# Kernel tuning notes

Hardware: AMD Instinct MI355X
Metric: run time of the kernel (lower is better)

## Reference

```python
import jax, jax.numpy as jnp
import numpy as np

B = 64        # number of graphs in the batch
NPG = 1024    # nodes per graph (uniform batch_num_nodes)
N = B * NPG   # total nodes = 65536
D = 512       # input feature dim
DEG = 32      # average degree
K = 0.5       # keep-percent
DROP = NPG - int(np.ceil(K * NPG))  # number of lowest-score nodes zeroed per graph


def setup_inputs() -> dict:
    key = jax.random.key(0)
    k1, k2, k3, k4 = jax.random.split(key, 4)
    features = jax.random.normal(k1, (N, D), dtype=jnp.float32)
    # edges constrained inside each graph's node block (batched DGL graph is block-diagonal)
    offsets = (jnp.arange(B, dtype=jnp.int64) * NPG)[:, None]
    src = (jax.random.randint(k2, (B, NPG * DEG), 0, NPG, dtype=jnp.int64) + offsets).reshape(-1)
    dst = (jax.random.randint(k3, (B, NPG * DEG), 0, NPG, dtype=jnp.int64) + offsets).reshape(-1)
    # GraphConv(input_dim=D, out=1) parameters (glorot-ish scale)
    weight = jax.random.normal(k4, (D, 1), dtype=jnp.float32) * (1.0 / np.sqrt(D))
    bias = jnp.zeros((1,), dtype=jnp.float32)
    return {"features": features, "src": src, "dst": dst, "weight": weight, "bias": bias}


def reference(features, src, dst, weight, bias):
    # --- GraphConv(D -> 1, norm=True, bias=True, activation=relu) ---
    # old-DGL norm=True: symmetric normalization with in-degrees, norm=deg^-0.5 (0 for isolated)
    deg = jnp.zeros((N,), features.dtype).at[dst].add(1.0)
    norm = jnp.where(deg > 0, deg ** -0.5, 0.0)[:, None]          # [N,1]
    # in_feats > out_feats: project first, then aggregate scalars
    h = (features @ weight) * norm                                # [N,1]
    agg = jnp.zeros_like(h).at[dst].add(h[src])                   # sum over in-edges
    w = jax.nn.relu(agg * norm + bias)                            # [N,1] scores
    # --- per-graph top-k masking: zero the DROP smallest scores in each graph ---
    wb = w.reshape(B, NPG)
    ranks = jnp.argsort(jnp.argsort(wb, axis=1), axis=1)          # rank 0 = smallest
    wb = jnp.where(ranks < DROP, jnp.zeros((), wb.dtype), wb)
    # --- elementwise gating of features by (masked) scores ---
    return features * wb.reshape(N, 1)
```

## Files before the change

kernel.cpp:

```cpp
#include <hip/hip_runtime.h>

#define NTOT 65536
#define DIM  512
#define BGR  64
#define NPG  1024
#define DROPN 512
#define SLICES 8

typedef float vf4 __attribute__((ext_vector_type(4)));

__global__ __launch_bounds__(256) void matvec_kernel(
        const float* __restrict__ X, const float* __restrict__ W,
        float* __restrict__ p) {
    const int lane = threadIdx.x & 63;
    const int nw   = (gridDim.x * blockDim.x) >> 6;
    const int wid  = (blockIdx.x * blockDim.x + threadIdx.x) >> 6;
    const vf4* wr = (const vf4*)W;
    const vf4 w0 = wr[lane], w1 = wr[lane + 64];
    for (int row = wid; row < NTOT; row += 2 * nw) {
        const int row2 = row + nw;
        const vf4* xr0 = (const vf4*)(X + (size_t)row  * DIM);
        const vf4* xr1 = (const vf4*)(X + (size_t)row2 * DIM);
        vf4 a0 = xr0[lane], a1 = xr0[lane + 64];
        vf4 b0 = xr1[lane], b1 = xr1[lane + 64];
        vf4 m0 = a0 * w0 + a1 * w1;
        vf4 m1 = b0 * w0 + b1 * w1;
        float s0 = m0[0] + m0[1] + m0[2] + m0[3];
        float s1 = m1[0] + m1[1] + m1[2] + m1[3];
        #pragma unroll
        for (int off = 32; off > 0; off >>= 1) {
            s0 += __shfl_down(s0, off, 64);
            s1 += __shfl_down(s1, off, 64);
        }
        if (lane == 0) { p[row] = s0; p[row2] = s1; }
    }
}

__global__ __launch_bounds__(256) void deg_partial_kernel(
        const int* __restrict__ dst, float* __restrict__ deg, int epg) {
    __shared__ int dl[NPG];
    const int g = blockIdx.x & (BGR - 1);
    const int slice = blockIdx.x >> 6;
    const int nbase = g * NPG;
    const int eps = epg / SLICES;
    for (int i = threadIdx.x; i < NPG; i += 256) dl[i] = 0;
    __syncthreads();
    const int4* d4 = (const int4*)(dst + (size_t)g * epg + (size_t)slice * eps);
    const int n4 = eps >> 2;
    for (int i = threadIdx.x; i < n4; i += 256) {
        int4 d = d4[i];
        atomicAdd(&dl[d.x - nbase], 1);
        atomicAdd(&dl[d.y - nbase], 1);
        atomicAdd(&dl[d.z - nbase], 1);
        atomicAdd(&dl[d.w - nbase], 1);
    }
    __syncthreads();
    for (int i = threadIdx.x; i < NPG; i += 256) {
        int c = dl[i];
        if (c) atomicAdd(&deg[nbase + i], (float)c);
    }
}

__global__ __launch_bounds__(256) void hn_kernel(
        const float* __restrict__ p, const float* __restrict__ deg,
        float* __restrict__ hn) {
    int i = blockIdx.x * blockDim.x + threadIdx.x;
    if (i < NTOT) {
        float d = deg[i];
        float nrm = d > 0.f ? (1.0f / sqrtf(d)) : 0.f;
        hn[i] = p[i] * nrm;
    }
}

__global__ __launch_bounds__(256) void agg_partial_kernel(
        const int* __restrict__ src, const int* __restrict__ dst,
        const float* __restrict__ hn, float* __restrict__ agg, int epg) {
    __shared__ float al[NPG];
    __shared__ float hl[NPG];
    const int g = blockIdx.x & (BGR - 1);
    const int slice = blockIdx.x >> 6;
    const int nbase = g * NPG;
    const int eps = epg / SLICES;
    for (int i = threadIdx.x; i < NPG; i += 256) {
        al[i] = 0.f;
        hl[i] = hn[nbase + i];
    }
    __syncthreads();
    const int4* s4 = (const int4*)(src + (size_t)g * epg + (size_t)slice * eps);
    const int4* d4 = (const int4*)(dst + (size_t)g * epg + (size_t)slice * eps);
    const int n4 = eps >> 2;
    for (int i = threadIdx.x; i < n4; i += 256) {
        int4 s = s4[i];
        int4 d = d4[i];
        atomicAdd(&al[d.x - nbase], hl[s.x - nbase]);
        atomicAdd(&al[d.y - nbase], hl[s.y - nbase]);
        atomicAdd(&al[d.z - nbase], hl[s.z - nbase]);
        atomicAdd(&al[d.w - nbase], hl[s.w - nbase]);
    }
    __syncthreads();
    for (int i = threadIdx.x; i < NPG; i += 256) {
        float v = al[i];
        if (v != 0.f) atomicAdd(&agg[nbase + i], v);
    }
}

__global__ __launch_bounds__(1024) void topk_kernel(
        const float* __restrict__ agg, const float* __restrict__ deg,
        const float* __restrict__ bias, float* __restrict__ gate) {
    __shared__ unsigned long long keys[NPG];
    __shared__ float wv[NPG];
    const int g = blockIdx.x;
    const int t = threadIdx.x;
    const int nbase = g * NPG;
    float d = deg[nbase + t];
    float nrm = d > 0.f ? (1.0f / sqrtf(d)) : 0.f;
    float w = agg[nbase + t] * nrm + bias[0];
    w = w > 0.f ? w : 0.f;
    wv[t] = w;
    keys[t] = ((unsigned long long)__float_as_uint(w) << 32) | (unsigned int)t;
    __syncthreads();
    for (int k = 2; k <= NPG; k <<= 1) {
        for (int j = k >> 1; j > 0; j >>= 1) {
            int ixj = t ^ j;
            if (ixj > t) {
                unsigned long long a = keys[t], c = keys[ixj];
                bool up = ((t & k) == 0);
                if ((a > c) == up) { keys[t] = c; keys[ixj] = a; }
            }
            __syncthreads();
        }
    }
    int idx = (int)(keys[t] & 0xffffffffull);
    gate[nbase + idx] = (t < DROPN) ? 0.f : wv[idx];
}

__global__ __launch_bounds__(256) void gate_kernel(
        const float* __restrict__ X, const float* __restrict__ gate,
        float* __restrict__ out) {
    const int lane = threadIdx.x & 63;
    const int nw   = (gridDim.x * blockDim.x) >> 6;
    const int wid  = (blockIdx.x * blockDim.x + threadIdx.x) >> 6;
    for (int row = wid; row < NTOT; row += nw) {
        float g = gate[__builtin_amdgcn_readfirstlane(row)];
        vf4* o = (vf4*)(out + (size_t)row * DIM);
        if (g == 0.f) {
            vf4 z = (vf4){0.f, 0.f, 0.f, 0.f};
            __builtin_nontemporal_store(z, &o[lane]);
            __builtin_nontemporal_store(z, &o[lane + 64]);
        } else {
            const vf4* xr = (const vf4*)(X + (size_t)row * DIM);
            vf4 a = xr[lane] * g;
            vf4 c = xr[lane + 64] * g;
            __builtin_nontemporal_store(a, &o[lane]);
            __builtin_nontemporal_store(c, &o[lane + 64]);
        }
    }
}

extern "C" void kernel_launch(void* const* d_in, const int* in_sizes, int n_in,
                              void* d_out, int out_size, void* d_ws, size_t ws_size,
                              hipStream_t stream) {
    const float* X    = (const float*)d_in[0];
    const int*   src  = (const int*)d_in[1];
    const int*   dst  = (const int*)d_in[2];
    const float* W    = (const float*)d_in[3];
    const float* bias = (const float*)d_in[4];
    float* out = (float*)d_out;
    int E   = in_sizes[1];
    int epg = E / BGR;

    float* ws   = (float*)d_ws;
    float* p    = ws;
    float* hn   = ws + 1 * NTOT;
    float* deg  = ws + 2 * NTOT;
    float* agg  = ws + 3 * NTOT;
    float* gate = ws + 4 * NTOT;

    hipMemsetAsync(deg, 0, 2 * NTOT * sizeof(float), stream);

    matvec_kernel<<<2048, 256, 0, stream>>>(X, W, p);
    deg_partial_kernel<<<BGR * SLICES, 256, 0, stream>>>(dst, deg, epg);
    hn_kernel<<<NTOT / 256, 256, 0, stream>>>(p, deg, hn);
    agg_partial_kernel<<<BGR * SLICES, 256, 0, stream>>>(src, dst, hn, agg, epg);
    topk_kernel<<<BGR, 1024, 0, stream>>>(agg, deg, bias, gate);
    gate_kernel<<<2048, 256, 0, stream>>>(X, gate, out);
}
```

Before: 284.9 us.

## Fuse pipeline into four kernels, replace atomics with slice partials, register bitonic sort

Merges the matvec and degree-count kernels into one launch, with separate block ranges for each job. Degree and aggregation partials are now written per slice and summed by the consumer, which removes the memset, the global atomics and the separate hn kernel. The top-k bitonic sort keeps keys in registers and uses wavefront shuffles for strides below 64, and the gate kernel switches from nontemporal stores to plain stores. This cuts launches and barriers, but adds reads of the partial buffers, and the change of store type may alter cache behaviour on the large output.

Result: no change. 280.2 us (-1.6%).

```diff
diff --git a/kernel.cpp b/kernel.cpp
--- a/kernel.cpp
+++ b/kernel.cpp
@@ -6,84 +6,81 @@
 #define NPG  1024
 #define DROPN 512
 #define SLICES 8
+#define MV_BLOCKS 2048
 
 typedef float vf4 __attribute__((ext_vector_type(4)));
+typedef unsigned long long u64;
 
-__global__ __launch_bounds__(256) void matvec_kernel(
+__global__ __launch_bounds__(256) void k1_matvec_deg(
         const float* __restrict__ X, const float* __restrict__ W,
-        float* __restrict__ p) {
-    const int lane = threadIdx.x & 63;
-    const int nw   = (gridDim.x * blockDim.x) >> 6;
-    const int wid  = (blockIdx.x * blockDim.x + threadIdx.x) >> 6;
-    const vf4* wr = (const vf4*)W;
-    const vf4 w0 = wr[lane], w1 = wr[lane + 64];
-    for (int row = wid; row < NTOT; row += 2 * nw) {
-        const int row2 = row + nw;
-        const vf4* xr0 = (const vf4*)(X + (size_t)row  * DIM);
-        const vf4* xr1 = (const vf4*)(X + (size_t)row2 * DIM);
-        vf4 a0 = xr0[lane], a1 = xr0[lane + 64];
-        vf4 b0 = xr1[lane], b1 = xr1[lane + 64];
-        vf4 m0 = a0 * w0 + a1 * w1;
-        vf4 m1 = b0 * w0 + b1 * w1;
-        float s0 = m0[0] + m0[1] + m0[2] + m0[3];
-        float s1 = m1[0] + m1[1] + m1[2] + m1[3];
-        #pragma unroll
-        for (int off = 32; off > 0; off >>= 1) {
-            s0 += __shfl_down(s0, off, 64);
-            s1 += __shfl_down(s1, off, 64);
+        const int* __restrict__ dst,
+        float* __restrict__ p, int* __restrict__ deg_part, int epg) {
+    __shared__ int dl[NPG];
+    if (blockIdx.x < MV_BLOCKS) {
+        const int lane = threadIdx.x & 63;
+        const int wid  = (blockIdx.x * 256 + threadIdx.x) >> 6;
+        const int nw   = (MV_BLOCKS * 256) >> 6;
+        const vf4* wr = (const vf4*)W;
+        const vf4 w0 = wr[lane], w1 = wr[lane + 64];
+        for (int row = wid; row < NTOT; row += 2 * nw) {
+            const int row2 = row + nw;
+            const vf4* xr0 = (const vf4*)(X + (size_t)row  * DIM);
+            const vf4* xr1 = (const vf4*)(X + (size_t)row2 * DIM);
+            vf4 a0 = xr0[lane], a1 = xr0[lane + 64];
+            vf4 b0 = xr1[lane], b1 = xr1[lane + 64];
+            vf4 m0 = a0 * w0 + a1 * w1;
+            vf4 m1 = b0 * w0 + b1 * w1;
+            float s0 = m0[0] + m0[1] + m0[2] + m0[3];
+            float s1 = m1[0] + m1[1] + m1[2] + m1[3];
+            #pragma unroll
+            for (int off = 32; off > 0; off >>= 1) {
+                s0 += __shfl_down(s0, off, 64);
+                s1 += __shfl_down(s1, off, 64);
+            }
+            if (lane == 0) { p[row] = s0; p[row2] = s1; }
         }
-        if (lane == 0) { p[row] = s0; p[row2] = s1; }
+    } else {
+        const int b = blockIdx.x - MV_BLOCKS;
+        const int g = b & (BGR - 1);
+        const int slice = b >> 6;
+        const int nbase = g * NPG;
+        const int eps = epg / SLICES;
+        for (int i = threadIdx.x; i < NPG; i += 256) dl[i] = 0;
+        __syncthreads();
+        const int4* d4 = (const int4*)(dst + (size_t)g * epg + (size_t)slice * eps);
+        const int n4 = eps >> 2;
+        for (int i = threadIdx.x; i < n4; i += 256) {
+            int4 d = d4[i];
+            atomicAdd(&dl[d.x - nbase], 1);
+            atomicAdd(&dl[d.y - nbase], 1);
+            atomicAdd(&dl[d.z - nbase], 1);
+            atomicAdd(&dl[d.w - nbase], 1);
+        }
+        __syncthreads();
+        int* out = deg_part + (size_t)slice * NTOT + nbase;
+        for (int i = threadIdx.x; i < NPG; i += 256) out[i] = dl[i];
     }
 }
 
-__global__ __launch_bounds__(256) void deg_partial_kernel(
-        const int* __restrict__ dst, float* __restrict__ deg, int epg) {
-    __shared__ int dl[NPG];
-    const int g = blockIdx.x & (BGR - 1);
-    const int slice = blockIdx.x >> 6;
-    const int nbase = g * NPG;
-    const int eps = epg / SLICES;
-    for (int i = threadIdx.x; i < NPG; i += 256) dl[i] = 0;
-    __syncthreads();
-    const int4* d4 = (const int4*)(dst + (size_t)g * epg + (size_t)slice * eps);
-    const int n4 = eps >> 2;
-    for (int i = threadIdx.x; i < n4; i += 256) {
-        int4 d = d4[i];
-        atomicAdd(&dl[d.x - nbase], 1);
-        atomicAdd(&dl[d.y - nbase], 1);
-        atomicAdd(&dl[d.z - nbase], 1);
-        atomicAdd(&dl[d.w - nbase], 1);
-    }
-    __syncthreads();
-    for (int i = threadIdx.x; i < NPG; i += 256) {
-        int c = dl[i];
-        if (c) atomicAdd(&deg[nbase + i], (float)c);
-    }
-}
-
-__global__ __launch_bounds__(256) void hn_kernel(
-        const float* __restrict__ p, const float* __restrict__ deg,
-        float* __restrict__ hn) {
-    int i = blockIdx.x * blockDim.x + threadIdx.x;
-    if (i < NTOT) {
-        float d = deg[i];
-        float nrm = d > 0.f ? (1.0f / sqrtf(d)) : 0.f;
-        hn[i] = p[i] * nrm;
-    }
-}
-
-__global__ __launch_bounds__(256) void agg_partial_kernel(
+__global__ __launch_bounds__(256) void k2_agg(
         const int* __restrict__ src, const int* __restrict__ dst,
-        const float* __restrict__ hn, float* __restrict__ agg, int epg) {
+        const float* __restrict__ p, const int* __restrict__ deg_part,
+        float* __restrict__ agg_part, float* __restrict__ norm_out, int epg) {
+    __shared__ float hl[NPG];
     __shared__ float al[NPG];
-    __shared__ float hl[NPG];
-    const int g = blockIdx.x & (BGR - 1);
-    const int slice = blockIdx.x >> 6;
+    const int b = blockIdx.x;
+    const int g = b & (BGR - 1);
+    const int slice = b >> 6;
     const int nbase = g * NPG;
     const int eps = epg / SLICES;
     for (int i = threadIdx.x; i < NPG; i += 256) {
+        int d = 0;
+        #pragma unroll
+        for (int s = 0; s < SLICES; s++) d += deg_part[(size_t)s * NTOT + nbase + i];
+        float nrm = d > 0 ? (1.0f / sqrtf((float)d)) : 0.f;
+        hl[i] = p[nbase + i] * nrm;
         al[i] = 0.f;
-        hl[i] = hn[nbase + i];
+        if (slice == 0) norm_out[nbase + i] = nrm;
     }
     __syncthreads();
     const int4* s4 = (const int4*)(src + (size_t)g * epg + (size_t)slice * eps);
@@ -98,61 +95,64 @@
         atomicAdd(&al[d.w - nbase], hl[s.w - nbase]);
     }
     __syncthreads();
-    for (int i = threadIdx.x; i < NPG; i += 256) {
-        float v = al[i];
-        if (v != 0.f) atomicAdd(&agg[nbase + i], v);
-    }
+    float* out = agg_part + (size_t)slice * NTOT + nbase;
+    for (int i = threadIdx.x; i < NPG; i += 256) out[i] = al[i];
 }
 
-__global__ __launch_bounds__(1024) void topk_kernel(
-        const float* __restrict__ agg, const float* __restrict__ deg,
+__global__ __launch_bounds__(1024) void k3_topk(
+        const float* __restrict__ agg_part, const float* __restrict__ norm,
         const float* __restrict__ bias, float* __restrict__ gate) {
-    __shared__ unsigned long long keys[NPG];
-    __shared__ float wv[NPG];
+    __shared__ u64 sk[NPG];
     const int g = blockIdx.x;
     const int t = threadIdx.x;
     const int nbase = g * NPG;
-    float d = deg[nbase + t];
-    float nrm = d > 0.f ? (1.0f / sqrtf(d)) : 0.f;
-    float w = agg[nbase + t] * nrm + bias[0];
+    float a = 0.f;
+    #pragma unroll
+    for (int s = 0; s < SLICES; s++) a += agg_part[(size_t)s * NTOT + nbase + t];
+    float w = a * norm[nbase + t] + bias[0];
     w = w > 0.f ? w : 0.f;
-    wv[t] = w;
-    keys[t] = ((unsigned long long)__float_as_uint(w) << 32) | (unsigned int)t;
-    __syncthreads();
+    u64 key = ((u64)__float_as_uint(w) << 32) | (unsigned int)t;
+
     for (int k = 2; k <= NPG; k <<= 1) {
-        for (int j = k >> 1; j > 0; j >>= 1) {
-            int ixj = t ^ j;
-            if (ixj > t) {
-                unsigned long long a = keys[t], c = keys[ixj];
-                bool up = ((t & k) == 0);
-                if ((a > c) == up) { keys[t] = c; keys[ixj] = a; }
-            }
+        const bool up = ((t & k) == 0);
+        for (int j = k >> 1; j >= 64; j >>= 1) {
+            sk[t] = key;
             __syncthreads();
+            u64 partner = sk[t ^ j];
+            __syncthreads();
+            bool takeMin = (((t & j) == 0) == up);
+            key = takeMin ? (key < partner ? key : partner)
+                          : (key > partner ? key : partner);
+        }
+        for (int j = ((k >> 1) < 32 ? (k >> 1) : 32); j >= 1; j >>= 1) {
+            u64 partner = (u64)__shfl_xor((long long)key, j, 64);
+            bool takeMin = (((t & j) == 0) == up);
+            key = takeMin ? (key < partner ? key : partner)
+                          : (key > partner ? key : partner);
         }
     }
-    int idx = (int)(keys[t] & 0xffffffffull);
-    gate[nbase + idx] = (t < DROPN) ? 0.f : wv[idx];
+    int idx = (int)(key & 0xffffffffull);
+    float wv = __uint_as_float((unsigned int)(key >> 32));
+    gate[nbase + idx] = (t < DROPN) ? 0.f : wv;
 }
 
-__global__ __launch_bounds__(256) void gate_kernel(
+__global__ __launch_bounds__(256) void k4_gate(
         const float* __restrict__ X, const float* __restrict__ gate,
         float* __restrict__ out) {
     const int lane = threadIdx.x & 63;
     const int nw   = (gridDim.x * blockDim.x) >> 6;
     const int wid  = (blockIdx.x * blockDim.x + threadIdx.x) >> 6;
     for (int row = wid; row < NTOT; row += nw) {
-        float g = gate[__builtin_amdgcn_readfirstlane(row)];
+        float g = gate[row];
         vf4* o = (vf4*)(out + (size_t)row * DIM);
         if (g == 0.f) {
             vf4 z = (vf4){0.f, 0.f, 0.f, 0.f};
-            __builtin_nontemporal_store(z, &o[lane]);
-            __builtin_nontemporal_store(z, &o[lane + 64]);
+            o[lane] = z;
+            o[lane + 64] = z;
         } else {
             const vf4* xr = (const vf4*)(X + (size_t)row * DIM);
-            vf4 a = xr[lane] * g;
-            vf4 c = xr[lane + 64] * g;
-            __builtin_nontemporal_store(a, &o[lane]);
-            __builtin_nontemporal_store(c, &o[lane + 64]);
+            o[lane]      = xr[lane] * g;
+            o[lane + 64] = xr[lane + 64] * g;
         }
     }
 }
@@ -169,19 +169,15 @@
     int E   = in_sizes[1];
     int epg = E / BGR;
 
-    float* ws   = (float*)d_ws;
-    float* p    = ws;
-    float* hn   = ws + 1 * NTOT;
-    float* deg  = ws + 2 * NTOT;
-    float* agg  = ws + 3 * NTOT;
-    float* gate = ws + 4 * NTOT;
+    float* ws       = (float*)d_ws;
+    float* p        = ws;
+    float* norm     = ws + 1 * NTOT;
+    float* gate     = ws + 2 * NTOT;
+    int*   deg_part = (int*)(ws + 3 * NTOT);
+    float* agg_part = ws + (3 + SLICES) * NTOT;
 
-    hipMemsetAsync(deg, 0, 2 * NTOT * sizeof(float), stream);
-
-    matvec_kernel<<<2048, 256, 0, stream>>>(X, W, p);
-    deg_partial_kernel<<<BGR * SLICES, 256, 0, stream>>>(dst, deg, epg);
-    hn_kernel<<<NTOT / 256, 256, 0, stream>>>(p, deg, hn);
-    agg_partial_kernel<<<BGR * SLICES, 256, 0, stream>>>(src, dst, hn, agg, epg);
-    topk_kernel<<<BGR, 1024, 0, stream>>>(agg, deg, bias, gate);
-    gate_kernel<<<2048, 256, 0, stream>>>(X, gate, out);
+    k1_matvec_deg<<<MV_BLOCKS + BGR * SLICES, 256, 0, stream>>>(X, W, dst, p, deg_part, epg);
+    k2_agg<<<BGR * SLICES, 256, 0, stream>>>(src, dst, p, deg_part, agg_part, norm, epg);
+    k3_topk<<<BGR, 1024, 0, stream>>>(agg_part, norm, bias, gate);
+    k4_gate<<<2048, 256, 0, stream>>>(X, gate, out);
 }
```
